# Kernel tuning notes

Measured on AMD Instinct MI355X. Metric: run time of the kernel, lower is better.

## Reference

```python
import jax, jax.numpy as jnp
import numpy as np

E = 8        # num_experts
K = 2        # top_k routing
D = 1024     # d_model
F = 4096     # expert hidden (ffn) dim
EPS = 1e-5


def _layernorm(h, g, b):
    # h: [E, T, C]; g, b: [E, C]
    mu = h.mean(axis=-1, keepdims=True)
    var = ((h - mu) ** 2).mean(axis=-1, keepdims=True)
    return (h - mu) * jax.lax.rsqrt(var + EPS) * g[:, None, :] + b[:, None, :]


def setup_inputs() -> dict:
    key = jax.random.key(0)
    ks = jax.random.split(key, 8)
    B, S = 2, 2048
    x = jax.random.normal(ks[0], (B, S, D), dtype=jnp.float32)
    Wr = jax.random.normal(ks[1], (D, E), dtype=jnp.float32) / np.sqrt(D)
    br = jnp.zeros((E,), dtype=jnp.float32)
    W1 = jax.random.normal(ks[2], (E, D, F), dtype=jnp.float32) / np.sqrt(D)
    b1 = jnp.zeros((E, F), dtype=jnp.float32)
    g1 = jnp.ones((E, F), dtype=jnp.float32)
    be1 = jnp.zeros((E, F), dtype=jnp.float32)
    W2 = jax.random.normal(ks[3], (E, F, D), dtype=jnp.float32) / np.sqrt(F)
    b2 = jnp.zeros((E, D), dtype=jnp.float32)
    g2 = jnp.ones((E, D), dtype=jnp.float32)
    be2 = jnp.zeros((E, D), dtype=jnp.float32)
    return {"x": x, "Wr": Wr, "br": br, "W1": W1, "b1": b1, "g1": g1,
            "be1": be1, "W2": W2, "b2": b2, "g2": g2, "be2": be2}


def reference(x, Wr, br, W1, b1, g1, be1, W2, b2, g2, be2):
    B, S, _ = x.shape
    xt = x.reshape(-1, D)                       # [T, D] token matrix
    # --- router + sampler: top-k softmax probs, renormalized over the k slots
    logits = xt @ Wr + br                       # [T, E]
    p = jax.nn.softmax(logits, axis=-1)
    probs, idx = jax.lax.top_k(p, K)            # [T, K]
    probs = probs / probs.sum(axis=-1, keepdims=True)
    # --- experts layer 1: Linear -> relu -> LayerNorm, per expert
    h = jnp.einsum('td,edf->etf', xt, W1) + b1[:, None, :]   # [E, T, F]
    h = _layernorm(jax.nn.relu(h), g1, be1)
    # --- experts layer 2: Linear -> relu -> LayerNorm
    y = jnp.einsum('etf,efd->etd', h, W2) + b2[:, None, :]   # [E, T, D]
    y = _layernorm(jax.nn.relu(y), g2, be2)
    # --- weighted scatter-combine: gate[t,e] = sum_k 1[idx[t,k]==e] * probs[t,k]
    gate = (jax.nn.one_hot(idx, E, dtype=x.dtype) * probs[..., None]).sum(axis=1)  # [T, E]
    out = jnp.einsum('te,etd->td', gate, y)     # index_add combine, dense form
    return out.reshape(B, S, D)
```

## Files before the change

kernel.cpp:

```cpp
#include <hip/hip_runtime.h>


#define E_N 8
#define TOPK 2
#define DM 1024
#define FF 4096
#define NTOK 4096
#define NA 8192
#define LN_EPS 1e-5f

typedef __attribute__((ext_vector_type(4))) float f32x4;
typedef __attribute__((ext_vector_type(8))) short short8;

__device__ __forceinline__ unsigned short f2bf(float f) {
    unsigned int u = __builtin_bit_cast(unsigned int, f);
    u = (u + 0x7FFFu + ((u >> 16) & 1u)) >> 16;
    return (unsigned short)u;
}
__device__ __forceinline__ float bf2f(unsigned short h) {
    unsigned int u = ((unsigned int)h) << 16;
    return __builtin_bit_cast(float, u);
}
__device__ __forceinline__ void unp(unsigned int u, float& lo, float& hi) {
    lo = bf2f((unsigned short)(u & 0xffffu));
    hi = bf2f((unsigned short)(u >> 16));
}
__device__ __forceinline__ unsigned int pk(float lo, float hi) {
    return (unsigned int)f2bf(lo) | ((unsigned int)f2bf(hi) << 16);
}

__device__ __forceinline__ void gload16(const unsigned short* g, unsigned short* lds) {
    __builtin_amdgcn_global_load_lds(
        (const __attribute__((address_space(1))) unsigned int*)g,
        (__attribute__((address_space(3))) unsigned int*)lds, 16, 0, 0);
}


__global__ __launch_bounds__(256) void k_prep(
        const float* __restrict__ W1, const float* __restrict__ W2,
        unsigned short* __restrict__ W1T, unsigned short* __restrict__ W2T,
        const float* __restrict__ x, const float* __restrict__ Wr,
        const float* __restrict__ br, unsigned short* __restrict__ xb,
        int* __restrict__ topk_idx, float* __restrict__ topk_p)
{
    __shared__ float tile[64][65];
    int z = blockIdx.z;
    int tid = threadIdx.x;

    if (z == 16) {
        int wv = tid >> 6, lane = tid & 63;
        int t = blockIdx.x * 4 + wv;
        const float* xr = x + (size_t)t * DM;
        unsigned short* xbr = xb + (size_t)t * DM;
        float a0=0,a1=0,a2=0,a3=0,a4=0,a5=0,a6=0,a7=0;
        for (int d = lane; d < DM; d += 64) {
            float xv = xr[d];
            xbr[d] = f2bf(xv);
            const float4* wp = (const float4*)(Wr + d * 8);
            float4 w0 = wp[0], w1 = wp[1];
            a0 += xv * w0.x; a1 += xv * w0.y; a2 += xv * w0.z; a3 += xv * w0.w;
            a4 += xv * w1.x; a5 += xv * w1.y; a6 += xv * w1.z; a7 += xv * w1.w;
        }
#pragma unroll
        for (int off = 32; off; off >>= 1) {
            a0 += __shfl_xor(a0, off); a1 += __shfl_xor(a1, off);
            a2 += __shfl_xor(a2, off); a3 += __shfl_xor(a3, off);
            a4 += __shfl_xor(a4, off); a5 += __shfl_xor(a5, off);
            a6 += __shfl_xor(a6, off); a7 += __shfl_xor(a7, off);
        }
        if (lane == 0) {
            float l[8] = {a0 + br[0], a1 + br[1], a2 + br[2], a3 + br[3],
                          a4 + br[4], a5 + br[5], a6 + br[6], a7 + br[7]};
            int i0 = 0;
#pragma unroll
            for (int e = 1; e < 8; e++) if (l[e] > l[i0]) i0 = e;
            int i1 = (i0 == 0) ? 1 : 0;
#pragma unroll
            for (int e = 0; e < 8; e++) if (e != i0 && l[e] > l[i1]) i1 = e;
            float p1 = expf(l[i1] - l[i0]);
            float s = 1.0f + p1;
            topk_idx[2 * t]     = i0;
            topk_idx[2 * t + 1] = i1;
            topk_p[2 * t]       = 1.0f / s;
            topk_p[2 * t + 1]   = p1 / s;
        }
        return;
    }

    const float* src; unsigned short* dst; int R, C, bx, by;
    if (z < 8) {
        R = DM; C = FF;
        src = W1 + (size_t)z * R * C;  dst = W1T + (size_t)z * R * C;
        bx = blockIdx.x & 63; by = blockIdx.x >> 6;
    } else {
        R = FF; C = DM;
        src = W2 + (size_t)(z - 8) * R * C;  dst = W2T + (size_t)(z - 8) * R * C;
        bx = blockIdx.x & 15; by = blockIdx.x >> 4;
    }
    const float* s = src + (size_t)(by * 64) * C + bx * 64;
    unsigned short* d = dst + (size_t)(bx * 64) * R + by * 64;
    int lr = tid >> 4, lc = (tid & 15) * 4;
#pragma unroll
    for (int p = 0; p < 4; p++) {
        float4 v = *(const float4*)(s + (size_t)(lr + p * 16) * C + lc);
        tile[lr + p * 16][lc] = v.x;     tile[lr + p * 16][lc + 1] = v.y;
        tile[lr + p * 16][lc + 2] = v.z; tile[lr + p * 16][lc + 3] = v.w;
    }
    __syncthreads();
    int rc = (tid & 7) * 8;
#pragma unroll
    for (int p = 0; p < 2; p++) {
        int cc = (tid >> 3) + p * 32;
        float a0 = tile[rc + 0][cc], a1 = tile[rc + 1][cc];
        float a2 = tile[rc + 2][cc], a3 = tile[rc + 3][cc];
        float a4 = tile[rc + 4][cc], a5 = tile[rc + 5][cc];
        float a6 = tile[rc + 6][cc], a7 = tile[rc + 7][cc];
        uint4 o;
        o.x = pk(a0, a1); o.y = pk(a2, a3); o.z = pk(a4, a5); o.w = pk(a6, a7);
        *(uint4*)(d + (size_t)cc * R + rc) = o;
    }
}


__global__ __launch_bounds__(256) void k_route2(const int* __restrict__ topk_idx,
        int* __restrict__ cnt, int* __restrict__ offs,
        int* __restrict__ assign_tok, int* __restrict__ assign_e,
        int* __restrict__ slot)
{
    __shared__ int h[8], base[8];
    int tid = threadIdx.x;
    if (tid < 8) h[tid] = 0;
    __syncthreads();
    int el[32];
#pragma unroll
    for (int i = 0; i < 32; i++) {
        int idx = tid * 32 + i;
        el[i] = topk_idx[idx];
        atomicAdd(&h[el[i]], 1);
    }
    __syncthreads();
    if (tid == 0) {
        int s = 0;
        for (int e = 0; e < E_N; e++) { offs[e] = s; cnt[e] = h[e]; base[e] = s; s += h[e]; }
        offs[E_N] = s;
    }
    __syncthreads();
    if (tid < 8) h[tid] = base[tid];
    __syncthreads();
#pragma unroll
    for (int i = 0; i < 32; i++) {
        int idx = tid * 32 + i;
        int e = el[i];
        int pos = atomicAdd(&h[e], 1);
        assign_tok[pos] = idx >> 1;
        assign_e[pos] = e;
        slot[idx] = pos;
    }
}


template<bool GATHER, bool EPI>
__global__ __launch_bounds__(256) void k_gemm(
    const unsigned short* __restrict__ A,
    const unsigned short* __restrict__ BT,
    const float* __restrict__ bias,
    unsigned short* __restrict__ C,
    const int* __restrict__ cnt, const int* __restrict__ offs,
    const int* __restrict__ gather_tok,
    int Kslice, int N, int ldA, int ldB, int GY, int GX, size_t slicePitch)
{
    __shared__ __align__(1024) char lds[32768];

    int bid = blockIdx.x;
    int e = bid & 7;
    int r = bid >> 3;
    int y = r % GY; r /= GY;
    int xn = r % GX;
    int ks = r / GX;

    int M = cnt[e];
    int m0 = y * 128;
    if (m0 >= M) return;
    int n0 = xn * 128;
    int off_e = offs[e];
    int kbase = ks * Kslice;
    int tid = threadIdx.x;
    int wv = tid >> 6, lane = tid & 63;
    int lr = lane & 15, hi = lane >> 4;
    int mW = (wv >> 1) * 64, nW = (wv & 1) * 64;

    int colsw = ((lane & 7) ^ (lane >> 3)) * 8;
    const unsigned short* aptr[4];
    const unsigned short* bptr[4];
#pragma unroll
    for (int i = 0; i < 4; i++) {
        int j = wv * 4 + i;
        int rr = m0 + j * 8 + (lane >> 3); rr = (rr < M) ? rr : (M - 1);
        size_t arow = GATHER ? (size_t)gather_tok[off_e + rr] : (size_t)(off_e + rr);
        aptr[i] = A + arow * (size_t)ldA + kbase + colsw;
        int rb = n0 + j * 8 + (lane >> 3);
        bptr[i] = BT + ((size_t)e * N + rb) * (size_t)ldB + kbase + colsw;
    }

    f32x4 acc[4][4];
    f32x4 zz = {0.f, 0.f, 0.f, 0.f};
#pragma unroll
    for (int mi = 0; mi < 4; mi++)
#pragma unroll
        for (int ni = 0; ni < 4; ni++) acc[mi][ni] = zz;

    int nt = Kslice >> 6;
    for (int t = 0; t < nt; ++t) {
        __syncthreads();
#pragma unroll
        for (int i = 0; i < 4; i++) {
            gload16(aptr[i] + t * 64, (unsigned short*)(lds + (wv * 4 + i) * 1024));
            gload16(bptr[i] + t * 64, (unsigned short*)(lds + 16384 + (wv * 4 + i) * 1024));
        }
        __syncthreads();
#pragma unroll
        for (int kss = 0; kss < 2; kss++) {
            int cb = (kss * 64 + hi * 16) ^ ((lr & 7) << 4);
            short8 afr[4], bfr[4];
#pragma unroll
            for (int ni = 0; ni < 4; ni++)
                bfr[ni] = *(const short8*)(lds + 16384 + (nW + ni * 16 + lr) * 128 + cb);
#pragma unroll
            for (int mi = 0; mi < 4; mi++)
                afr[mi] = *(const short8*)(lds + (mW + mi * 16 + lr) * 128 + cb);
            __builtin_amdgcn_s_setprio(1);
#pragma unroll
            for (int mi = 0; mi < 4; mi++)
#pragma unroll
                for (int ni = 0; ni < 4; ni++)
                    acc[mi][ni] = __builtin_amdgcn_mfma_f32_16x16x32_bf16(
                        afr[mi], bfr[ni], acc[mi][ni], 0, 0, 0);
            __builtin_amdgcn_s_setprio(0);
        }
    }

    unsigned short* Cs = C + ks * slicePitch;
    float bv[4] = {0.f, 0.f, 0.f, 0.f};
    if (EPI) {
#pragma unroll
        for (int ni = 0; ni < 4; ni++)
            bv[ni] = bias[(size_t)e * N + (n0 + nW + ni * 16 + lr)];
    }
#pragma unroll
    for (int mi = 0; mi < 4; mi++) {
        int mb = m0 + mW + mi * 16 + hi * 4;
#pragma unroll
        for (int rr = 0; rr < 4; rr++) {
            int m = mb + rr;
            if (m < M) {
                unsigned short* crow = Cs + (size_t)(off_e + m) * N;
#pragma unroll
                for (int ni = 0; ni < 4; ni++) {
                    float v = acc[mi][ni][rr];
                    if (EPI) v = fmaxf(v + bv[ni], 0.0f);
                    crow[n0 + nW + ni * 16 + lr] = f2bf(v);
                }
            }
        }
    }
}


__global__ __launch_bounds__(256) void k_ln1(unsigned short* __restrict__ H,
        const float* __restrict__ g, const float* __restrict__ b,
        const int* __restrict__ assign_e)
{
    size_t a = blockIdx.x;
    int e = assign_e[a];
    unsigned short* row = H + a * FF;
    int tid = threadIdx.x;
    uint4 u0 = *(const uint4*)(row + tid * 16);
    uint4 u1 = *(const uint4*)(row + tid * 16 + 8);
    float v[16];
    unp(u0.x, v[0], v[1]);  unp(u0.y, v[2], v[3]);
    unp(u0.z, v[4], v[5]);  unp(u0.w, v[6], v[7]);
    unp(u1.x, v[8], v[9]);  unp(u1.y, v[10], v[11]);
    unp(u1.z, v[12], v[13]); unp(u1.w, v[14], v[15]);
    float s = 0.f, q = 0.f;
#pragma unroll
    for (int i = 0; i < 16; i++) { s += v[i]; q += v[i] * v[i]; }
#pragma unroll
    for (int off = 32; off; off >>= 1) { s += __shfl_xor(s, off); q += __shfl_xor(q, off); }
    __shared__ float red[8];
    int wv = tid >> 6, lane = tid & 63;
    if (lane == 0) { red[wv * 2] = s; red[wv * 2 + 1] = q; }
    __syncthreads();
    s = red[0] + red[2] + red[4] + red[6];
    q = red[1] + red[3] + red[5] + red[7];
    float mu = s * (1.0f / FF);
    float var = q * (1.0f / FF) - mu * mu;
    float rstd = rsqrtf(var + LN_EPS);
    const float* gg = g + (size_t)e * FF + tid * 16;
    const float* bb = b + (size_t)e * FF + tid * 16;
    float4 G0 = *(const float4*)(gg);      float4 G1 = *(const float4*)(gg + 4);
    float4 G2 = *(const float4*)(gg + 8);  float4 G3 = *(const float4*)(gg + 12);
    float4 B0 = *(const float4*)(bb);      float4 B1 = *(const float4*)(bb + 4);
    float4 B2 = *(const float4*)(bb + 8);  float4 B3 = *(const float4*)(bb + 12);
    float gvv[16] = {G0.x,G0.y,G0.z,G0.w,G1.x,G1.y,G1.z,G1.w,G2.x,G2.y,G2.z,G2.w,G3.x,G3.y,G3.z,G3.w};
    float bvv[16] = {B0.x,B0.y,B0.z,B0.w,B1.x,B1.y,B1.z,B1.w,B2.x,B2.y,B2.z,B2.w,B3.x,B3.y,B3.z,B3.w};
#pragma unroll
    for (int i = 0; i < 16; i++) v[i] = (v[i] - mu) * rstd * gvv[i] + bvv[i];
    u0.x = pk(v[0], v[1]);  u0.y = pk(v[2], v[3]);
    u0.z = pk(v[4], v[5]);  u0.w = pk(v[6], v[7]);
    u1.x = pk(v[8], v[9]);  u1.y = pk(v[10], v[11]);
    u1.z = pk(v[12], v[13]); u1.w = pk(v[14], v[15]);
    *(uint4*)(row + tid * 16) = u0;
    *(uint4*)(row + tid * 16 + 8) = u1;
}


__global__ __launch_bounds__(256) void k_comb(const unsigned short* __restrict__ Yp,
        const float* __restrict__ g, const float* __restrict__ b2,
        const float* __restrict__ be,
        const int* __restrict__ slot, const float* __restrict__ topk_p,
        const int* __restrict__ assign_e, float* __restrict__ out)
{
    int t = blockIdx.x;
    int s0 = slot[2 * t], s1 = slot[2 * t + 1];
    float p0 = topk_p[2 * t], p1 = topk_p[2 * t + 1];
    int e0 = assign_e[s0], e1 = assign_e[s1];
    int tid = threadIdx.x;
    int d = tid * 4;
    const unsigned short* Y1 = Yp + (size_t)NA * DM;
    uint2 ua0 = *(const uint2*)(Yp + (size_t)s0 * DM + d);
    uint2 ua1 = *(const uint2*)(Y1 + (size_t)s0 * DM + d);
    uint2 ub0 = *(const uint2*)(Yp + (size_t)s1 * DM + d);
    uint2 ub1 = *(const uint2*)(Y1 + (size_t)s1 * DM + d);
    float4 bza = *(const float4*)(b2 + (size_t)e0 * DM + d);
    float4 bzb = *(const float4*)(b2 + (size_t)e1 * DM + d);
    float x0, x1, y0, y1;
    float va[4], vb[4];
    unp(ua0.x, x0, x1); unp(ua1.x, y0, y1);
    va[0] = fmaxf(x0 + y0 + bza.x, 0.f); va[1] = fmaxf(x1 + y1 + bza.y, 0.f);
    unp(ua0.y, x0, x1); unp(ua1.y, y0, y1);
    va[2] = fmaxf(x0 + y0 + bza.z, 0.f); va[3] = fmaxf(x1 + y1 + bza.w, 0.f);
    unp(ub0.x, x0, x1); unp(ub1.x, y0, y1);
    vb[0] = fmaxf(x0 + y0 + bzb.x, 0.f); vb[1] = fmaxf(x1 + y1 + bzb.y, 0.f);
    unp(ub0.y, x0, x1); unp(ub1.y, y0, y1);
    vb[2] = fmaxf(x0 + y0 + bzb.z, 0.f); vb[3] = fmaxf(x1 + y1 + bzb.w, 0.f);

    float sa = 0.f, qa = 0.f, sb = 0.f, qb = 0.f;
#pragma unroll
    for (int i = 0; i < 4; i++) {
        sa += va[i]; qa += va[i] * va[i];
        sb += vb[i]; qb += vb[i] * vb[i];
    }
#pragma unroll
    for (int off = 32; off; off >>= 1) {
        sa += __shfl_xor(sa, off); qa += __shfl_xor(qa, off);
        sb += __shfl_xor(sb, off); qb += __shfl_xor(qb, off);
    }
    __shared__ float red[16];
    int wv = tid >> 6, lane = tid & 63;
    if (lane == 0) { red[wv*4+0]=sa; red[wv*4+1]=qa; red[wv*4+2]=sb; red[wv*4+3]=qb; }
    __syncthreads();
    sa = red[0] + red[4] + red[8]  + red[12];
    qa = red[1] + red[5] + red[9]  + red[13];
    sb = red[2] + red[6] + red[10] + red[14];
    qb = red[3] + red[7] + red[11] + red[15];
    float mua = sa * (1.0f / DM), vara = qa * (1.0f / DM) - mua * mua;
    float ra = rsqrtf(vara + LN_EPS);
    float mub = sb * (1.0f / DM), varb = qb * (1.0f / DM) - mub * mub;
    float rb = rsqrtf(varb + LN_EPS);
    float4 ga  = *(const float4*)(g + (size_t)e0 * DM + d);
    float4 ba  = *(const float4*)(be + (size_t)e0 * DM + d);
    float4 gb4 = *(const float4*)(g + (size_t)e1 * DM + d);
    float4 bb4 = *(const float4*)(be + (size_t)e1 * DM + d);
    float4 o;
    o.x = p0 * ((va[0] - mua) * ra * ga.x + ba.x) + p1 * ((vb[0] - mub) * rb * gb4.x + bb4.x);
    o.y = p0 * ((va[1] - mua) * ra * ga.y + ba.y) + p1 * ((vb[1] - mub) * rb * gb4.y + bb4.y);
    o.z = p0 * ((va[2] - mua) * ra * ga.z + ba.z) + p1 * ((vb[2] - mub) * rb * gb4.z + bb4.z);
    o.w = p0 * ((va[3] - mua) * ra * ga.w + ba.w) + p1 * ((vb[3] - mub) * rb * gb4.w + bb4.w);
    *(float4*)(out + (size_t)t * DM + d) = o;
}


extern "C" void kernel_launch(void* const* d_in, const int* in_sizes, int n_in,
                              void* d_out, int out_size, void* d_ws, size_t ws_size,
                              hipStream_t stream) {
    const float* x   = (const float*)d_in[0];
    const float* Wr  = (const float*)d_in[1];
    const float* br  = (const float*)d_in[2];
    const float* W1  = (const float*)d_in[3];
    const float* b1  = (const float*)d_in[4];
    const float* g1  = (const float*)d_in[5];
    const float* be1 = (const float*)d_in[6];
    const float* W2  = (const float*)d_in[7];
    const float* b2  = (const float*)d_in[8];
    const float* g2  = (const float*)d_in[9];
    const float* be2 = (const float*)d_in[10];
    float* out = (float*)d_out;

    char* w = (char*)d_ws;
    int*   cnt        = (int*)(w);
    int*   offs       = (int*)(w + 128);
    int*   topk_idx   = (int*)(w + 512);
    float* topk_p     = (float*)(w + 512 + (32 << 10));
    int*   assign_tok = (int*)(w + 512 + (64 << 10));
    int*   assign_e   = (int*)(w + 512 + (96 << 10));
    int*   slot       = (int*)(w + 512 + (128 << 10));
    unsigned short* xb  = (unsigned short*)(w + ((size_t)1 << 20));
    unsigned short* W1T = (unsigned short*)(w + ((size_t)9 << 20));
    unsigned short* W2T = (unsigned short*)(w + ((size_t)73 << 20));
    unsigned short* Hb  = (unsigned short*)(w + ((size_t)137 << 20));
    unsigned short* Yp  = (unsigned short*)(w + ((size_t)201 << 20));

    k_prep<<<dim3(1024, 1, 17), 256, 0, stream>>>(
        W1, W2, W1T, W2T, x, Wr, br, xb, topk_idx, topk_p);
    k_route2<<<1, 256, 0, stream>>>(topk_idx, cnt, offs, assign_tok, assign_e, slot);
    k_gemm<true, true><<<8 * 32 * 32, 256, 0, stream>>>(
        xb, W1T, b1, Hb, cnt, offs, assign_tok, DM, FF, DM, DM, 32, 32, 0);
    k_ln1<<<NA, 256, 0, stream>>>(Hb, g1, be1, assign_e);
    k_gemm<false, false><<<8 * 32 * 8 * 2, 256, 0, stream>>>(
        Hb, W2T, nullptr, Yp, cnt, offs, nullptr, FF / 2, DM, FF, FF, 32, 8,
        (size_t)NA * DM);
    k_comb<<<NTOK, 256, 0, stream>>>(Yp, g2, b2, be2, slot, topk_p, assign_e, out);
}
```

Before: 374.4 us.

## Make expert GEMMs persistent with per-expert tile loops instead of oversized grids

Replaces the fixed worst-case grid (one block per possible 128-row tile, most exiting early) with 128 persistent blocks per expert that stride over that expert's actual tile count (rows × column tiles × K slices). It also adds a min-blocks-per-SM hint of 4 to launch_bounds. The aim is to remove the launch and scheduling cost of many empty blocks. In exchange, load balance across experts is fixed by the per-expert block count, so a heavily loaded expert gets no extra blocks, and the occupancy hint may constrain register allocation.

```diff
diff --git a/kernel.cpp b/kernel.cpp
--- a/kernel.cpp
+++ b/kernel.cpp
@@ -8,6 +8,7 @@
 #define NTOK 4096
 #define NA 8192
 #define LN_EPS 1e-5f
+#define NBX 128
 
 typedef __attribute__((ext_vector_type(4))) float f32x4;
 typedef __attribute__((ext_vector_type(8))) short short8;
@@ -160,105 +161,112 @@
 
 
 template<bool GATHER, bool EPI>
-__global__ __launch_bounds__(256) void k_gemm(
+__global__ __launch_bounds__(256, 4) void k_gemm(
     const unsigned short* __restrict__ A,
     const unsigned short* __restrict__ BT,
     const float* __restrict__ bias,
     unsigned short* __restrict__ C,
     const int* __restrict__ cnt, const int* __restrict__ offs,
     const int* __restrict__ gather_tok,
-    int Kslice, int N, int ldA, int ldB, int GY, int GX, size_t slicePitch)
+    int Kslice, int N, int ldA, int ldB, int GX, int KS, size_t slicePitch)
 {
     __shared__ __align__(1024) char lds[32768];
 
     int bid = blockIdx.x;
     int e = bid & 7;
-    int r = bid >> 3;
-    int y = r % GY; r /= GY;
-    int xn = r % GX;
-    int ks = r / GX;
-
+    int lb = bid >> 3;
     int M = cnt[e];
-    int m0 = y * 128;
-    if (m0 >= M) return;
-    int n0 = xn * 128;
+    if (M <= 0) return;
     int off_e = offs[e];
-    int kbase = ks * Kslice;
+    int nrows = (M + 127) >> 7;
+    int ntiles = nrows * GX * KS;
+
     int tid = threadIdx.x;
     int wv = tid >> 6, lane = tid & 63;
     int lr = lane & 15, hi = lane >> 4;
     int mW = (wv >> 1) * 64, nW = (wv & 1) * 64;
-
     int colsw = ((lane & 7) ^ (lane >> 3)) * 8;
-    const unsigned short* aptr[4];
-    const unsigned short* bptr[4];
-#pragma unroll
-    for (int i = 0; i < 4; i++) {
-        int j = wv * 4 + i;
-        int rr = m0 + j * 8 + (lane >> 3); rr = (rr < M) ? rr : (M - 1);
-        size_t arow = GATHER ? (size_t)gather_tok[off_e + rr] : (size_t)(off_e + rr);
-        aptr[i] = A + arow * (size_t)ldA + kbase + colsw;
-        int rb = n0 + j * 8 + (lane >> 3);
-        bptr[i] = BT + ((size_t)e * N + rb) * (size_t)ldB + kbase + colsw;
-    }
-
-    f32x4 acc[4][4];
-    f32x4 zz = {0.f, 0.f, 0.f, 0.f};
-#pragma unroll
-    for (int mi = 0; mi < 4; mi++)
-#pragma unroll
-        for (int ni = 0; ni < 4; ni++) acc[mi][ni] = zz;
-
+    int l3 = lane >> 3;
     int nt = Kslice >> 6;
-    for (int t = 0; t < nt; ++t) {
-        __syncthreads();
+
+    for (int t = lb; t < ntiles; t += NBX) {
+        int r = t % nrows;
+        int q = t / nrows;
+        int xn = q % GX;
+        int ks = q / GX;
+        int m0 = r * 128;
+        int n0 = xn * 128;
+        int kbase = ks * Kslice;
+
+        const unsigned short* aptr[4];
+        const unsigned short* bptr[4];
 #pragma unroll
         for (int i = 0; i < 4; i++) {
-            gload16(aptr[i] + t * 64, (unsigned short*)(lds + (wv * 4 + i) * 1024));
-            gload16(bptr[i] + t * 64, (unsigned short*)(lds + 16384 + (wv * 4 + i) * 1024));
-        }
-        __syncthreads();
-#pragma unroll
-        for (int kss = 0; kss < 2; kss++) {
-            int cb = (kss * 64 + hi * 16) ^ ((lr & 7) << 4);
-            short8 afr[4], bfr[4];
+            int j = wv * 4 + i;
+            int rr = m0 + j * 8 + l3; rr = (rr < M) ? rr : (M - 1);
+            size_t arow = GATHER ? (size_t)gather_tok[off_e + rr] : (size_t)(off_e + rr);
+            aptr[i] = A + arow * (size_t)ldA + kbase + colsw;
+            int rb = n0 + j * 8 + l3;
+            bptr[i] = BT + ((size_t)e * N + rb) * (size_t)ldB + kbase + colsw;
+        }
+
+        f32x4 acc[4][4];
+        f32x4 zz = {0.f, 0.f, 0.f, 0.f};
+#pragma unroll
+        for (int mi = 0; mi < 4; mi++)
+#pragma unroll
+            for (int ni = 0; ni < 4; ni++) acc[mi][ni] = zz;
+
+        for (int kt = 0; kt < nt; ++kt) {
+            __syncthreads();
+#pragma unroll
+            for (int i = 0; i < 4; i++) {
+                gload16(aptr[i] + kt * 64, (unsigned short*)(lds + (wv * 4 + i) * 1024));
+                gload16(bptr[i] + kt * 64, (unsigned short*)(lds + 16384 + (wv * 4 + i) * 1024));
+            }
+            __syncthreads();
+#pragma unroll
+            for (int kss = 0; kss < 2; kss++) {
+                int cb = (kss * 64 + hi * 16) ^ ((lr & 7) << 4);
+                short8 afr[4], bfr[4];
+#pragma unroll
+                for (int ni = 0; ni < 4; ni++)
+                    bfr[ni] = *(const short8*)(lds + 16384 + (nW + ni * 16 + lr) * 128 + cb);
+#pragma unroll
+                for (int mi = 0; mi < 4; mi++)
+                    afr[mi] = *(const short8*)(lds + (mW + mi * 16 + lr) * 128 + cb);
+                __builtin_amdgcn_s_setprio(1);
+#pragma unroll
+                for (int mi = 0; mi < 4; mi++)
+#pragma unroll
+                    for (int ni = 0; ni < 4; ni++)
+                        acc[mi][ni] = __builtin_amdgcn_mfma_f32_16x16x32_bf16(
+                            afr[mi], bfr[ni], acc[mi][ni], 0, 0, 0);
+                __builtin_amdgcn_s_setprio(0);
+            }
+        }
+
+        unsigned short* Cs = C + ks * slicePitch;
+        float bv[4] = {0.f, 0.f, 0.f, 0.f};
+        if (EPI) {
 #pragma unroll
             for (int ni = 0; ni < 4; ni++)
-                bfr[ni] = *(const short8*)(lds + 16384 + (nW + ni * 16 + lr) * 128 + cb);
-#pragma unroll
-            for (int mi = 0; mi < 4; mi++)
-                afr[mi] = *(const short8*)(lds + (mW + mi * 16 + lr) * 128 + cb);
-            __builtin_amdgcn_s_setprio(1);
-#pragma unroll
-            for (int mi = 0; mi < 4; mi++)
-#pragma unroll
-                for (int ni = 0; ni < 4; ni++)
-                    acc[mi][ni] = __builtin_amdgcn_mfma_f32_16x16x32_bf16(
-                        afr[mi], bfr[ni], acc[mi][ni], 0, 0, 0);
-            __builtin_amdgcn_s_setprio(0);
-        }
-    }
-
-    unsigned short* Cs = C + ks * slicePitch;
-    float bv[4] = {0.f, 0.f, 0.f, 0.f};
-    if (EPI) {
-#pragma unroll
-        for (int ni = 0; ni < 4; ni++)
-            bv[ni] = bias[(size_t)e * N + (n0 + nW + ni * 16 + lr)];
-    }
-#pragma unroll
-    for (int mi = 0; mi < 4; mi++) {
-        int mb = m0 + mW + mi * 16 + hi * 4;
-#pragma unroll
-        for (int rr = 0; rr < 4; rr++) {
-            int m = mb + rr;
-            if (m < M) {
-                unsigned short* crow = Cs + (size_t)(off_e + m) * N;
-#pragma unroll
-                for (int ni = 0; ni < 4; ni++) {
-                    float v = acc[mi][ni][rr];
-                    if (EPI) v = fmaxf(v + bv[ni], 0.0f);
-                    crow[n0 + nW + ni * 16 + lr] = f2bf(v);
+                bv[ni] = bias[(size_t)e * N + (n0 + nW + ni * 16 + lr)];
+        }
+#pragma unroll
+        for (int mi = 0; mi < 4; mi++) {
+            int mb = m0 + mW + mi * 16 + hi * 4;
+#pragma unroll
+            for (int rr = 0; rr < 4; rr++) {
+                int m = mb + rr;
+                if (m < M) {
+                    unsigned short* crow = Cs + (size_t)(off_e + m) * N;
+#pragma unroll
+                    for (int ni = 0; ni < 4; ni++) {
+                        float v = acc[mi][ni][rr];
+                        if (EPI) v = fmaxf(v + bv[ni], 0.0f);
+                        crow[n0 + nW + ni * 16 + lr] = f2bf(v);
+                    }
                 }
             }
         }
@@ -413,11 +421,11 @@
     k_prep<<<dim3(1024, 1, 17), 256, 0, stream>>>(
         W1, W2, W1T, W2T, x, Wr, br, xb, topk_idx, topk_p);
     k_route2<<<1, 256, 0, stream>>>(topk_idx, cnt, offs, assign_tok, assign_e, slot);
-    k_gemm<true, true><<<8 * 32 * 32, 256, 0, stream>>>(
-        xb, W1T, b1, Hb, cnt, offs, assign_tok, DM, FF, DM, DM, 32, 32, 0);
+    k_gemm<true, true><<<8 * NBX, 256, 0, stream>>>(
+        xb, W1T, b1, Hb, cnt, offs, assign_tok, DM, FF, DM, DM, 32, 1, 0);
     k_ln1<<<NA, 256, 0, stream>>>(Hb, g1, be1, assign_e);
-    k_gemm<false, false><<<8 * 32 * 8 * 2, 256, 0, stream>>>(
-        Hb, W2T, nullptr, Yp, cnt, offs, nullptr, FF / 2, DM, FF, FF, 32, 8,
+    k_gemm<false, false><<<8 * NBX, 256, 0, stream>>>(
+        Hb, W2T, nullptr, Yp, cnt, offs, nullptr, FF / 2, DM, FF, FF, 8, 2,
         (size_t)NA * DM);
     k_comb<<<NTOK, 256, 0, stream>>>(Yp, g2, b2, be2, slot, topk_p, assign_e, out);
 }
```

New measurement: 333.1 us. 11.0% less time.
